# Kernel tuning notes

Measured on AMD Instinct MI355X. Metric: run time of the kernel, lower is better.

## Reference

```python
import jax, jax.numpy as jnp
import numpy as np
import math

B, P, C, D, H = 4, 2048, 512, 1024, 16
DH = D // H
EPS = 1e-6


def setup_inputs() -> dict:
    key = jax.random.key(0)
    ks = jax.random.split(key, 10)
    para = jax.random.normal(ks[0], (B, P, D), dtype=jnp.float32)
    cluster = jax.random.normal(ks[1], (B, C, D), dtype=jnp.float32)
    e = jax.random.uniform(ks[2], (B, P, C), dtype=jnp.float32)
    edge = jnp.where(e > 0.5, e, 0.0)
    s = 1.0 / math.sqrt(D)
    Wq = jax.random.uniform(ks[3], (D, D), jnp.float32, -s, s)
    bq = jnp.zeros((D,), jnp.float32)
    Wk = jax.random.uniform(ks[4], (D, D), jnp.float32, -s, s)
    bk = jnp.zeros((D,), jnp.float32)
    Wv = jax.random.uniform(ks[5], (D, D), jnp.float32, -s, s)
    bv = jnp.zeros((D,), jnp.float32)
    gamma = jnp.ones((D,), jnp.float32)
    beta = jnp.zeros((D,), jnp.float32)
    return {"para": para, "cluster": cluster, "edge": edge,
            "Wq": Wq, "bq": bq, "Wk": Wk, "bk": bk, "Wv": Wv, "bv": bv,
            "gamma": gamma, "beta": beta}


def reference(para, cluster, edge, Wq, bq, Wk, bk, Wv, bv, gamma, beta):
    # projections: [B, L, D] -> [B, H, L, DH]
    def shape(x):
        b, l, _ = x.shape
        return x.reshape(b, l, H, DH).transpose(0, 2, 1, 3)

    q = shape(para @ Wq + bq) / math.sqrt(DH)   # [B,H,P,DH]
    k = shape(cluster @ Wk + bk)                # [B,H,C,DH]
    v = shape(cluster @ Wv + bv)                # [B,H,C,DH]

    scores = jnp.einsum('bhpd,bhcd->bhpc', q, k)  # [B,H,P,C]
    mask = (edge > 0)[:, None, :, :]              # broadcast over heads
    scores = jnp.where(mask, scores, -1e18)
    attn = jax.nn.softmax(scores, axis=-1)
    attn = attn * edge[:, None, :, :]             # post-softmax edge weighting
    # dropout is identity at inference
    ctx = jnp.einsum('bhpc,bhcd->bhpd', attn, v)  # [B,H,P,DH]
    ctx = ctx.transpose(0, 2, 1, 3).reshape(B, P, D)
    # LayerNorm(model_dim), eps=1e-6
    mu = jnp.mean(ctx, axis=-1, keepdims=True)
    var = jnp.mean(jnp.square(ctx - mu), axis=-1, keepdims=True)
    out = (ctx - mu) * jax.lax.rsqrt(var + EPS) * gamma + beta
    return out
```

## Files before the change

kernel.cpp:

```cpp
#include <hip/hip_runtime.h>

#define BB 4
#define PP 2048
#define CCLUS 512
#define DD 1024
#define HH 16
#define DHH 64

typedef __attribute__((ext_vector_type(8))) short short8;
typedef __attribute__((ext_vector_type(4))) float floatx4;
typedef unsigned short u16;
typedef unsigned int u32;
typedef unsigned long long u64;

__device__ __forceinline__ float bf2f(u16 u) {
  union { u32 i; float f; } v; v.i = ((u32)u) << 16; return v.f;
}
__device__ __forceinline__ u16 f2bf(float f) {
  union { float f; u32 i; } v; v.f = f;
  u32 x = v.i;
  return (u16)((x + 0x7fffu + ((x >> 16) & 1u)) >> 16);
}
__device__ __forceinline__ u64 pack4(float a, float b, float c, float d) {
  return (u64)f2bf(a) | ((u64)f2bf(b) << 16) | ((u64)f2bf(c) << 32) | ((u64)f2bf(d) << 48);
}

__device__ __forceinline__ floatx4 mfma16(short8 a, short8 b, floatx4 c) {
  return __builtin_amdgcn_mfma_f32_16x16x32_bf16(a, b, c, 0, 0, 0);
}

__device__ __forceinline__ void gload_lds16(const u16* g, u16* l) {
  __builtin_amdgcn_global_load_lds(
      (const __attribute__((address_space(1))) u32*)g,
      (__attribute__((address_space(3))) u32*)l, 16, 0, 0);
}

__global__ __launch_bounds__(256) void cast_k(
    const float* __restrict__ para, const float* __restrict__ cluster,
    u16* __restrict__ Ap, u16* __restrict__ Ac) {
  const int NP4 = (BB * PP * DD) / 4;
  const int NC4 = (BB * CCLUS * DD) / 4;
  const int stride = gridDim.x * blockDim.x;
  for (int i = blockIdx.x * blockDim.x + threadIdx.x; i < NP4 + NC4; i += stride) {
    const float* src; u16* dst; int j;
    if (i < NP4) { src = para; dst = Ap; j = i; }
    else         { src = cluster; dst = Ac; j = i - NP4; }
    const float4 v = *(const float4*)(src + (size_t)j * 4);
    *(u64*)(dst + (size_t)j * 4) = pack4(v.x, v.y, v.z, v.w);
  }
}

__global__ __launch_bounds__(1024) void transpose3_k(
    const float* __restrict__ Wq, const float* __restrict__ Wk, const float* __restrict__ Wv,
    u16* __restrict__ WqT, u16* __restrict__ WkT, u16* __restrict__ WvT) {
  __shared__ u16 tile[32][33];
  const int z = blockIdx.z;
  const float* src = (z == 0) ? Wq : (z == 1) ? Wk : Wv;
  u16* dst = (z == 0) ? WqT : (z == 1) ? WkT : WvT;
  int x = blockIdx.x * 32 + threadIdx.x;
  int y = blockIdx.y * 32 + threadIdx.y;
  tile[threadIdx.y][threadIdx.x] = f2bf(src[y * DD + x]);
  __syncthreads();
  x = blockIdx.y * 32 + threadIdx.x;
  y = blockIdx.x * 32 + threadIdx.y;
  dst[y * DD + x] = tile[threadIdx.x][threadIdx.y];
}

__global__ __launch_bounds__(256) void qkv_gemm3(
    const u16* __restrict__ Ap, const u16* __restrict__ Ac,
    const u16* __restrict__ WqT, const u16* __restrict__ WkT, const u16* __restrict__ WvT,
    const float* __restrict__ bq, const float* __restrict__ bk, const float* __restrict__ bv,
    u16* __restrict__ Qb, u16* __restrict__ Kp, u16* __restrict__ Vt) {
  const int bx = blockIdx.x;
  const u16* A; const u16* BT; const float* bias; int mt, mode;
  if (bx < 64)      { A = Ap; BT = WqT; bias = bq; mt = bx;      mode = 0; }
  else if (bx < 80) { A = Ac; BT = WkT; bias = bk; mt = bx - 64; mode = 1; }
  else              { A = Ac; BT = WvT; bias = bv; mt = bx - 80; mode = 2; }

  __shared__ __align__(16) u16 As[128 * 32];
  __shared__ __align__(16) u16 Bs[128 * 32];

  const int tid = threadIdx.x;
  const int w = tid >> 6, lane = tid & 63, quad = lane >> 4, cidx = lane & 15;
  const int wy = w >> 1, wx = w & 1;
  const int m0 = mt * 128, n0 = blockIdx.y * 128;

  floatx4 acc[4][4];
#pragma unroll
  for (int i = 0; i < 4; i++)
#pragma unroll
    for (int j = 0; j < 4; j++) acc[i][j] = (floatx4){0.f, 0.f, 0.f, 0.f};

  const int row0 = tid >> 2, kc0 = tid & 3;
  const int offG0 = row0 * 1024 + kc0 * 8;
  const int offG1 = (row0 + 64) * 1024 + kc0 * 8;
  u16* ldsA0 = As + (size_t)(w * 64) * 8;
  u16* ldsA1 = As + (size_t)(w * 64 + 256) * 8;
  u16* ldsB0 = Bs + (size_t)(w * 64) * 8;
  u16* ldsB1 = Bs + (size_t)(w * 64 + 256) * 8;

  const u16* Abase = A + (size_t)m0 * 1024;
  const u16* Bbase = BT + (size_t)n0 * 1024;

  for (int kt = 0; kt < 32; kt++) {
    const u16* Ak = Abase + kt * 32;
    const u16* Bk = Bbase + kt * 32;
    gload_lds16(Ak + offG0, ldsA0);
    gload_lds16(Ak + offG1, ldsA1);
    gload_lds16(Bk + offG0, ldsB0);
    gload_lds16(Bk + offG1, ldsB1);
    __syncthreads();

    short8 af[4], bfr[4];
#pragma unroll
    for (int i = 0; i < 4; i++) {
      int ra = wy * 64 + i * 16 + cidx;
      af[i] = *(const short8*)&As[ra * 32 + quad * 8];
      int rb = wx * 64 + i * 16 + cidx;
      bfr[i] = *(const short8*)&Bs[rb * 32 + quad * 8];
    }
#pragma unroll
    for (int mi = 0; mi < 4; mi++)
#pragma unroll
      for (int ni = 0; ni < 4; ni++)
        acc[mi][ni] = mfma16(af[mi], bfr[ni], acc[mi][ni]);
    __syncthreads();
  }

#pragma unroll
  for (int ni = 0; ni < 4; ni++) {
    const int ncol = n0 + wx * 64 + ni * 16 + cidx;
    const float bvv = bias[ncol];
    const int h = ncol >> 6, dh = ncol & 63;
#pragma unroll
    for (int mi = 0; mi < 4; mi++) {
      const int mrow = m0 + wy * 64 + mi * 16 + quad * 4;
      if (mode == 0) {
#pragma unroll
        for (int r = 0; r < 4; r++) {
          float v = (acc[mi][ni][r] + bvv) * 0.125f;
          Qb[(size_t)(mrow + r) * 1024 + ncol] = f2bf(v);
        }
      } else if (mode == 1) {
#pragma unroll
        for (int r = 0; r < 4; r++) {
          const int row = mrow + r;
          const int bb = row >> 9, c = row & 511;
          Kp[((size_t)(bb * HH + h) * CCLUS + c) * DHH + dh] = f2bf(acc[mi][ni][r] + bvv);
        }
      } else {
        const int bb = mrow >> 9, c0 = mrow & 511;
        *(u64*)&Vt[((size_t)(bb * HH + h) * DHH + dh) * CCLUS + c0] =
            pack4(acc[mi][ni][0] + bvv, acc[mi][ni][1] + bvv,
                  acc[mi][ni][2] + bvv, acc[mi][ni][3] + bvv);
      }
    }
  }
}

__global__ __launch_bounds__(512, 5) void attn_k4(
    const u16* __restrict__ Qb, const u16* __restrict__ Kp, const u16* __restrict__ Vt,
    const float* __restrict__ edge, float* __restrict__ ctx) {
  const int b = blockIdx.z, h = blockIdx.y, p0 = blockIdx.x * 128;
  const int tid = threadIdx.x;
  const int w = tid >> 6, lane = tid & 63, quad = lane >> 4, cidx = lane & 15;

  __shared__ __align__(16) u16 Ks[2][64 * 64];
  __shared__ __align__(16) u16 Vs[2][64 * 64];
  __shared__ __align__(16) u16 attnS[8][16][72];

  const u16* __restrict__ Kbh = Kp + (size_t)(b * HH + h) * CCLUS * DHH;
  const u16* __restrict__ Vbh = Vt + (size_t)(b * HH + h) * DHH * CCLUS;

  const int prow = p0 + w * 16 + cidx;
  const u16* qg = Qb + (size_t)(b * PP + prow) * DD + h * DHH + quad * 8;
  const short8 qf0 = *(const short8*)qg;
  const short8 qf1 = *(const short8*)(qg + 32);
  const float* Erow = edge + (size_t)(b * PP + prow) * CCLUS;

  float srow = 0.f;
  floatx4 oacc[4];
#pragma unroll
  for (int nt = 0; nt < 4; nt++) oacc[nt] = (floatx4){0.f, 0.f, 0.f, 0.f};

  const int srow_i = tid >> 3;
  const int sc = ((tid & 7) ^ (srow_i & 7)) << 3;
  const int ldsoff = w * 64 * 8;

  auto STAGE = [&](int cc, int bufi) {
    const u16* kg = Kbh + (size_t)cc * 64 * DHH;
    const u16* vg = Vbh + cc * 64;
    gload_lds16(kg + (size_t)srow_i * DHH + sc, &Ks[bufi][ldsoff]);
    gload_lds16(vg + (size_t)srow_i * CCLUS + sc, &Vs[bufi][ldsoff]);
  };

  STAGE(0, 0);
  __syncthreads();

  const int swz = (cidx & 7) << 3;

  for (int cc = 0; cc < 8; cc++) {
    const int bufi = cc & 1;
    if (cc < 7) STAGE(cc + 1, bufi ^ 1);
    const u16* __restrict__ KsB = &Ks[bufi][0];
    const u16* __restrict__ VsB = &Vs[bufi][0];

#pragma unroll
    for (int t = 0; t < 4; t++) {
      const int krow = (t * 16 + cidx) * 64;
      const short8 kf0 = *(const short8*)&KsB[krow + ((quad * 8) ^ swz)];
      const short8 kf1 = *(const short8*)&KsB[krow + ((32 + quad * 8) ^ swz)];
      floatx4 s4 = (floatx4){0.f, 0.f, 0.f, 0.f};
      s4 = mfma16(kf0, qf0, s4);
      s4 = mfma16(kf1, qf1, s4);
      const int ce = cc * 64 + t * 16 + quad * 4;
      const float4 e4 = *(const float4*)(Erow + ce);
      float E[4];
#pragma unroll
      for (int r = 0; r < 4; r++) {
        const float e = (&e4.x)[r];
        const float sv = s4[r];
        const float ex = (e > 0.f && sv == sv) ? __expf(fminf(sv, 15.f)) : 0.f;
        srow += ex;
        E[r] = ex * e;
      }
      *(u64*)&attnS[w][cidx][t * 16 + quad * 4] = pack4(E[0], E[1], E[2], E[3]);
    }
#pragma unroll
    for (int ks = 0; ks < 2; ks++) {
      const short8 afr = *(const short8*)&attnS[w][cidx][ks * 32 + quad * 8];
#pragma unroll
      for (int nt = 0; nt < 4; nt++) {
        const short8 bfr =
            *(const short8*)&VsB[(nt * 16 + cidx) * 64 + ((ks * 32 + quad * 8) ^ swz)];
        oacc[nt] = mfma16(afr, bfr, oacc[nt]);
      }
    }
    __syncthreads();
  }

  srow += __shfl_xor(srow, 16, 64);
  srow += __shfl_xor(srow, 32, 64);
  const float sinv = (srow > 0.f) ? 1.0f / srow : 0.f;

#pragma unroll
  for (int r = 0; r < 4; r++) {
    const float sv = __shfl(sinv, quad * 4 + r, 16);
#pragma unroll
    for (int nt = 0; nt < 4; nt++) {
      const size_t off =
          (size_t)(b * PP + p0 + w * 16 + quad * 4 + r) * DD + h * DHH + nt * 16 + cidx;
      ctx[off] = oacc[nt][r] * sv;
    }
  }
}

__global__ __launch_bounds__(256) void ln_k(
    float* buf, const float* __restrict__ gamma, const float* __restrict__ beta) {
  const int row = blockIdx.x, tid = threadIdx.x;
  const int w = tid >> 6, lane = tid & 63;
  float* x = buf + (size_t)row * DD + tid * 4;
  float4 v = *(const float4*)x;
  float s = v.x + v.y + v.z + v.w;
  float sq = v.x * v.x + v.y * v.y + v.z * v.z + v.w * v.w;
#pragma unroll
  for (int off = 1; off < 64; off <<= 1) {
    s += __shfl_xor(s, off, 64);
    sq += __shfl_xor(sq, off, 64);
  }
  __shared__ float red[8];
  if (lane == 0) { red[w] = s; red[4 + w] = sq; }
  __syncthreads();
  s = red[0] + red[1] + red[2] + red[3];
  sq = red[4] + red[5] + red[6] + red[7];
  const float mu = s * (1.f / 1024.f);
  const float var = sq * (1.f / 1024.f) - mu * mu;
  const float rs = rsqrtf(fmaxf(var, 0.f) + 1e-6f);
  const float4 gr = *(const float4*)(gamma + tid * 4);
  const float4 br = *(const float4*)(beta + tid * 4);
  float4 y;
  y.x = (v.x - mu) * rs * gr.x + br.x;
  y.y = (v.y - mu) * rs * gr.y + br.y;
  y.z = (v.z - mu) * rs * gr.z + br.z;
  y.w = (v.w - mu) * rs * gr.w + br.w;
  *(float4*)x = y;
}

extern "C" void kernel_launch(void* const* d_in, const int* in_sizes, int n_in,
                              void* d_out, int out_size, void* d_ws, size_t ws_size,
                              hipStream_t stream) {
  const float* para    = (const float*)d_in[0];
  const float* cluster = (const float*)d_in[1];
  const float* edge    = (const float*)d_in[2];
  const float* Wq      = (const float*)d_in[3];
  const float* bq      = (const float*)d_in[4];
  const float* Wk      = (const float*)d_in[5];
  const float* bk      = (const float*)d_in[6];
  const float* Wv      = (const float*)d_in[7];
  const float* bv      = (const float*)d_in[8];
  const float* gamma   = (const float*)d_in[9];
  const float* beta    = (const float*)d_in[10];
  float* out = (float*)d_out;

  u16* WqT = (u16*)d_ws;
  u16* WkT = WqT + (size_t)1024 * 1024;
  u16* WvT = WkT + (size_t)1024 * 1024;
  u16* Qb  = WvT + (size_t)1024 * 1024;
  u16* Kp  = Qb  + (size_t)8192 * 1024;
  u16* Vt  = Kp  + (size_t)2048 * 1024;
  u16* Ap  = Vt  + (size_t)2048 * 1024;
  u16* Ac  = Ap  + (size_t)8192 * 1024;

  cast_k<<<dim3(2048), dim3(256), 0, stream>>>(para, cluster, Ap, Ac);
  transpose3_k<<<dim3(32, 32, 3), dim3(32, 32), 0, stream>>>(Wq, Wk, Wv, WqT, WkT, WvT);
  qkv_gemm3<<<dim3(96, 8), dim3(256), 0, stream>>>(Ap, Ac, WqT, WkT, WvT,
                                                   bq, bk, bv, Qb, Kp, Vt);
  attn_k4<<<dim3(PP / 128, HH, BB), dim3(512), 0, stream>>>(Qb, Kp, Vt, edge, out);
  ln_k<<<dim3(BB * PP), dim3(256), 0, stream>>>(out, gamma, beta);
}
```

Measured before the change: 245.5 us.

## Keep softmax probabilities in registers via permlane swaps and use native exp2

The attention kernel no longer writes the bf16 probability tile to shared memory and reads it back. It packs the probabilities with v_cvt_pk_bf16_f32 and rearranges them into the MFMA A-operand layout with permlane32/16 swaps. Q is prescaled by log2(e)/8 so the raw v_exp_f32 (exp2) instruction can be used, and setprio hints are added around the MFMA blocks. V is now written row-major by the GEMM and transposed in a separate small kernel, which adds an extra launch and an extra pass over V in exchange for coalesced GEMM stores; the occupancy hint is also raised.

```diff
diff --git a/kernel.cpp b/kernel.cpp
--- a/kernel.cpp
+++ b/kernel.cpp
@@ -20,9 +20,6 @@
   union { float f; u32 i; } v; v.f = f;
   u32 x = v.i;
   return (u16)((x + 0x7fffu + ((x >> 16) & 1u)) >> 16);
-}
-__device__ __forceinline__ u64 pack4(float a, float b, float c, float d) {
-  return (u64)f2bf(a) | ((u64)f2bf(b) << 16) | ((u64)f2bf(c) << 32) | ((u64)f2bf(d) << 48);
 }
 
 __device__ __forceinline__ floatx4 mfma16(short8 a, short8 b, floatx4 c) {
@@ -46,7 +43,9 @@
     if (i < NP4) { src = para; dst = Ap; j = i; }
     else         { src = cluster; dst = Ac; j = i - NP4; }
     const float4 v = *(const float4*)(src + (size_t)j * 4);
-    *(u64*)(dst + (size_t)j * 4) = pack4(v.x, v.y, v.z, v.w);
+    u64 p = (u64)f2bf(v.x) | ((u64)f2bf(v.y) << 16) | ((u64)f2bf(v.z) << 32) |
+            ((u64)f2bf(v.w) << 48);
+    *(u64*)(dst + (size_t)j * 4) = p;
   }
 }
 
@@ -70,12 +69,12 @@
     const u16* __restrict__ Ap, const u16* __restrict__ Ac,
     const u16* __restrict__ WqT, const u16* __restrict__ WkT, const u16* __restrict__ WvT,
     const float* __restrict__ bq, const float* __restrict__ bk, const float* __restrict__ bv,
-    u16* __restrict__ Qb, u16* __restrict__ Kp, u16* __restrict__ Vt) {
+    u16* __restrict__ Qb, u16* __restrict__ Kp, u16* __restrict__ Vb) {
   const int bx = blockIdx.x;
-  const u16* A; const u16* BT; const float* bias; int mt, mode;
-  if (bx < 64)      { A = Ap; BT = WqT; bias = bq; mt = bx;      mode = 0; }
-  else if (bx < 80) { A = Ac; BT = WkT; bias = bk; mt = bx - 64; mode = 1; }
-  else              { A = Ac; BT = WvT; bias = bv; mt = bx - 80; mode = 2; }
+  const u16* A; const u16* BT; const float* bias; u16* Cout; float scale; int mt, mode;
+  if (bx < 64)      { A = Ap; BT = WqT; bias = bq; Cout = Qb; scale = 0.18033688f; mt = bx;      mode = 0; }
+  else if (bx < 80) { A = Ac; BT = WkT; bias = bk; Cout = 0;  scale = 1.0f;        mt = bx - 64; mode = 1; }
+  else              { A = Ac; BT = WvT; bias = bv; Cout = Vb; scale = 1.0f;        mt = bx - 80; mode = 2; }
 
   __shared__ __align__(16) u16 As[128 * 32];
   __shared__ __align__(16) u16 Bs[128 * 32];
@@ -131,34 +130,55 @@
   for (int ni = 0; ni < 4; ni++) {
     const int ncol = n0 + wx * 64 + ni * 16 + cidx;
     const float bvv = bias[ncol];
-    const int h = ncol >> 6, dh = ncol & 63;
 #pragma unroll
     for (int mi = 0; mi < 4; mi++) {
       const int mrow = m0 + wy * 64 + mi * 16 + quad * 4;
-      if (mode == 0) {
-#pragma unroll
-        for (int r = 0; r < 4; r++) {
-          float v = (acc[mi][ni][r] + bvv) * 0.125f;
-          Qb[(size_t)(mrow + r) * 1024 + ncol] = f2bf(v);
-        }
-      } else if (mode == 1) {
+      if (mode == 1) {
+        const int hh2 = ncol >> 6, dh = ncol & 63;
 #pragma unroll
         for (int r = 0; r < 4; r++) {
           const int row = mrow + r;
           const int bb = row >> 9, c = row & 511;
-          Kp[((size_t)(bb * HH + h) * CCLUS + c) * DHH + dh] = f2bf(acc[mi][ni][r] + bvv);
+          Kp[((size_t)(bb * HH + hh2) * CCLUS + c) * DHH + dh] = f2bf(acc[mi][ni][r] + bvv);
         }
       } else {
-        const int bb = mrow >> 9, c0 = mrow & 511;
-        *(u64*)&Vt[((size_t)(bb * HH + h) * DHH + dh) * CCLUS + c0] =
-            pack4(acc[mi][ni][0] + bvv, acc[mi][ni][1] + bvv,
-                  acc[mi][ni][2] + bvv, acc[mi][ni][3] + bvv);
+#pragma unroll
+        for (int r = 0; r < 4; r++) {
+          float v = (acc[mi][ni][r] + bvv) * scale;
+          Cout[(size_t)(mrow + r) * 1024 + ncol] = f2bf(v);
+        }
       }
     }
   }
 }
 
-__global__ __launch_bounds__(512, 5) void attn_k4(
+__global__ __launch_bounds__(256) void vt_k(
+    const u16* __restrict__ Vb, u16* __restrict__ Vt) {
+  __shared__ u16 t[64][72];
+  const int ct = blockIdx.x;
+  const int bh = blockIdx.y;
+  const int b = bh >> 4, h = bh & 15;
+  const int tid = threadIdx.x;
+#pragma unroll
+  for (int pass = 0; pass < 2; pass++) {
+    int idx = pass * 256 + tid;
+    int c = idx >> 3, d0 = (idx & 7) * 8;
+    short8 v = *(const short8*)&Vb[(size_t)(b * 512 + ct * 64 + c) * 1024 + h * 64 + d0];
+    *(short8*)&t[c][d0] = v;
+  }
+  __syncthreads();
+#pragma unroll
+  for (int pass = 0; pass < 2; pass++) {
+    int idx = pass * 256 + tid;
+    int d = idx >> 3, c0 = (idx & 7) * 8;
+    short8 o;
+#pragma unroll
+    for (int j = 0; j < 8; j++) ((u16*)&o)[j] = t[c0 + j][d];
+    *(short8*)&Vt[((size_t)(bh) * 64 + d) * 512 + ct * 64 + c0] = o;
+  }
+}
+
+__global__ __launch_bounds__(512, 8) void attn_k5(
     const u16* __restrict__ Qb, const u16* __restrict__ Kp, const u16* __restrict__ Vt,
     const float* __restrict__ edge, float* __restrict__ ctx) {
   const int b = blockIdx.z, h = blockIdx.y, p0 = blockIdx.x * 128;
@@ -167,7 +187,6 @@
 
   __shared__ __align__(16) u16 Ks[2][64 * 64];
   __shared__ __align__(16) u16 Vs[2][64 * 64];
-  __shared__ __align__(16) u16 attnS[8][16][72];
 
   const u16* __restrict__ Kbh = Kp + (size_t)(b * HH + h) * CCLUS * DHH;
   const u16* __restrict__ Vbh = Vt + (size_t)(b * HH + h) * DHH * CCLUS;
@@ -185,7 +204,7 @@
 
   const int srow_i = tid >> 3;
   const int sc = ((tid & 7) ^ (srow_i & 7)) << 3;
-  const int ldsoff = w * 64 * 8;
+  const int ldsoff = w * 512;
 
   auto STAGE = [&](int cc, int bufi) {
     const u16* kg = Kbh + (size_t)cc * 64 * DHH;
@@ -206,35 +225,49 @@
     const u16* __restrict__ VsB = &Vs[bufi][0];
 
 #pragma unroll
-    for (int t = 0; t < 4; t++) {
-      const int krow = (t * 16 + cidx) * 64;
-      const short8 kf0 = *(const short8*)&KsB[krow + ((quad * 8) ^ swz)];
-      const short8 kf1 = *(const short8*)&KsB[krow + ((32 + quad * 8) ^ swz)];
-      floatx4 s4 = (floatx4){0.f, 0.f, 0.f, 0.f};
-      s4 = mfma16(kf0, qf0, s4);
-      s4 = mfma16(kf1, qf1, s4);
-      const int ce = cc * 64 + t * 16 + quad * 4;
-      const float4 e4 = *(const float4*)(Erow + ce);
-      float E[4];
-#pragma unroll
-      for (int r = 0; r < 4; r++) {
-        const float e = (&e4.x)[r];
-        const float sv = s4[r];
-        const float ex = (e > 0.f && sv == sv) ? __expf(fminf(sv, 15.f)) : 0.f;
-        srow += ex;
-        E[r] = ex * e;
+    for (int ks = 0; ks < 2; ks++) {
+      u32 pa[2], pb[2];
+#pragma unroll
+      for (int tt = 0; tt < 2; tt++) {
+        const int t = ks * 2 + tt;
+        const int krow = (t * 16 + cidx) * 64;
+        const short8 kf0 = *(const short8*)&KsB[krow + ((quad * 8) ^ swz)];
+        const short8 kf1 = *(const short8*)&KsB[krow + ((32 + quad * 8) ^ swz)];
+        floatx4 s4 = (floatx4){0.f, 0.f, 0.f, 0.f};
+        __builtin_amdgcn_s_setprio(1);
+        s4 = mfma16(kf0, qf0, s4);
+        s4 = mfma16(kf1, qf1, s4);
+        __builtin_amdgcn_s_setprio(0);
+        const int ce = cc * 64 + t * 16 + quad * 4;
+        const float4 e4 = *(const float4*)(Erow + ce);
+        float E[4];
+#pragma unroll
+        for (int r = 0; r < 4; r++) {
+          const float e = (&e4.x)[r];
+          float x = fminf(s4[r], 21.6f);
+          float ex;
+          asm("v_exp_f32 %0, %1\n\ts_nop 0" : "=v"(ex) : "v"(x));
+          ex = (e > 0.f) ? ex : 0.f;
+          srow += ex;
+          E[r] = ex * e;
+        }
+        asm("v_cvt_pk_bf16_f32 %0, %1, %2" : "=v"(pa[tt]) : "v"(E[0]), "v"(E[1]));
+        asm("v_cvt_pk_bf16_f32 %0, %1, %2" : "=v"(pb[tt]) : "v"(E[2]), "v"(E[3]));
       }
-      *(u64*)&attnS[w][cidx][t * 16 + quad * 4] = pack4(E[0], E[1], E[2], E[3]);
-    }
-#pragma unroll
-    for (int ks = 0; ks < 2; ks++) {
-      const short8 afr = *(const short8*)&attnS[w][cidx][ks * 32 + quad * 8];
+      asm("v_permlane32_swap_b32 %0, %1" : "+v"(pa[0]), "+v"(pa[1]));
+      asm("v_permlane16_swap_b32 %0, %1" : "+v"(pa[0]), "+v"(pa[1]));
+      asm("v_permlane32_swap_b32 %0, %1" : "+v"(pb[0]), "+v"(pb[1]));
+      asm("v_permlane16_swap_b32 %0, %1" : "+v"(pb[0]), "+v"(pb[1]));
+      union { u32 u[4]; short8 s; } af;
+      af.u[0] = pa[0]; af.u[1] = pb[0]; af.u[2] = pa[1]; af.u[3] = pb[1];
+      __builtin_amdgcn_s_setprio(1);
 #pragma unroll
       for (int nt = 0; nt < 4; nt++) {
         const short8 bfr =
             *(const short8*)&VsB[(nt * 16 + cidx) * 64 + ((ks * 32 + quad * 8) ^ swz)];
-        oacc[nt] = mfma16(afr, bfr, oacc[nt]);
+        oacc[nt] = mfma16(af.s, bfr, oacc[nt]);
       }
+      __builtin_amdgcn_s_setprio(0);
     }
     __syncthreads();
   }
@@ -310,11 +343,13 @@
   u16* Vt  = Kp  + (size_t)2048 * 1024;
   u16* Ap  = Vt  + (size_t)2048 * 1024;
   u16* Ac  = Ap  + (size_t)8192 * 1024;
+  u16* Vb  = Ac  + (size_t)2048 * 1024;
 
   cast_k<<<dim3(2048), dim3(256), 0, stream>>>(para, cluster, Ap, Ac);
   transpose3_k<<<dim3(32, 32, 3), dim3(32, 32), 0, stream>>>(Wq, Wk, Wv, WqT, WkT, WvT);
   qkv_gemm3<<<dim3(96, 8), dim3(256), 0, stream>>>(Ap, Ac, WqT, WkT, WvT,
-                                                   bq, bk, bv, Qb, Kp, Vt);
-  attn_k4<<<dim3(PP / 128, HH, BB), dim3(512), 0, stream>>>(Qb, Kp, Vt, edge, out);
+                                                   bq, bk, bv, Qb, Kp, Vb);
+  vt_k<<<dim3(8, 64), dim3(256), 0, stream>>>(Vb, Vt);
+  attn_k5<<<dim3(PP / 128, HH, BB), dim3(512), 0, stream>>>(Qb, Kp, Vt, edge, out);
   ln_k<<<dim3(BB * PP), dim3(256), 0, stream>>>(out, gamma, beta);
 }
```

Result: faster. 226.4 us (-7.8%).
